# Kernel optimization log

Measured on AMD Instinct MI355X. Metric: run time of the kernel, lower is better.

Reference implementation:

```python
import jax, jax.numpy as jnp
import numpy as np

FEATURE_DIMS = [4, 4, 4, 4, 4, 4, 4, 4, 4, 4, 4, 4, 2, 2, 1, 4, 1, 1, 1, 1, 1, 1, 2]
FEATURE_AMOUNT = len(FEATURE_DIMS)  # 23
EMBEDDING_DIM = 10
KQ_DIM = 10
OBS_SPACE = int(np.sum(FEATURE_DIMS))  # 65
BATCH = 131072


def _block_mask():
    # Block-diagonal mask: feature i's input slice maps only to its own 10-dim embedding.
    m = np.zeros((OBS_SPACE, FEATURE_AMOUNT * EMBEDDING_DIM), dtype=np.float32)
    r = 0
    for i, d in enumerate(FEATURE_DIMS):
        m[r:r + d, i * EMBEDDING_DIM:(i + 1) * EMBEDDING_DIM] = 1.0
        r += d
    return jnp.asarray(m)

PROJ_MASK = _block_mask()


def setup_inputs() -> dict:
    key = jax.random.key(0)
    ks = jax.random.split(key, 24)
    s = 0.1  # weight scale for numerically sane softmax
    inp = {
        "x": jax.random.normal(ks[0], (BATCH, OBS_SPACE), jnp.float32),
        "W_proj": jax.random.normal(ks[1], (OBS_SPACE, FEATURE_AMOUNT * EMBEDDING_DIM), jnp.float32) * s,
        "b_proj": jax.random.normal(ks[2], (FEATURE_AMOUNT * EMBEDDING_DIM,), jnp.float32) * s,
        "Wq": jax.random.normal(ks[3], (EMBEDDING_DIM, KQ_DIM), jnp.float32) * s,
        "Wk": jax.random.normal(ks[4], (EMBEDDING_DIM, KQ_DIM), jnp.float32) * s,
        "Wv": jax.random.normal(ks[5], (EMBEDDING_DIM, EMBEDDING_DIM), jnp.float32) * s,
        "W1": jax.random.normal(ks[6], (FEATURE_AMOUNT * EMBEDDING_DIM, 164), jnp.float32) * s,
        "b1": jax.random.normal(ks[7], (164,), jnp.float32) * s,
        "W2": jax.random.normal(ks[8], (164, 164), jnp.float32) * s,
        "b2": jax.random.normal(ks[9], (164,), jnp.float32) * s,
        "W3": jax.random.normal(ks[10], (164, 164), jnp.float32) * s,
        "b3": jax.random.normal(ks[11], (164,), jnp.float32) * s,
        "W4": jax.random.normal(ks[12], (164, 164), jnp.float32) * s,
        "b4": jax.random.normal(ks[13], (164,), jnp.float32) * s,
        "W5": jax.random.normal(ks[14], (164, 164), jnp.float32) * s,
        "b5": jax.random.normal(ks[15], (164,), jnp.float32) * s,
        "W_move": jax.random.normal(ks[16], (164, 5), jnp.float32) * 0.01,
        "b_move": jax.random.normal(ks[17], (5,), jnp.float32) * s,
        "W_mark": jax.random.normal(ks[18], (164, 1), jnp.float32) * 0.01,
        "b_mark": jax.random.normal(ks[19], (1,), jnp.float32) * s,
    }
    return inp


def reference(x, W_proj, b_proj, Wq, Wk, Wv, W1, b1, W2, b2, W3, b3, W4, b4, W5, b5,
              W_move, b_move, W_mark, b_mark):
    # Projection: 23 tiny Linears fused as one block-diagonal GEMM. [B,65] -> [B,23,10]
    h = (x @ (W_proj * PROJ_MASK) + b_proj).reshape(-1, FEATURE_AMOUNT, EMBEDDING_DIM)
    # Tiny self-attention over the 23 feature tokens.
    q = h @ Wq  # [B,23,kq]
    k = h @ Wk  # [B,23,kq]
    v = h @ Wv  # [B,23,10]
    logits = jnp.einsum('bid,bjd->bij', q, k) / np.float32(np.sqrt(KQ_DIM))
    omega = jax.nn.softmax(logits, axis=-1)
    ctx = jnp.einsum('bij,bjd->bid', omega, v)
    z = (h + ctx).reshape(-1, FEATURE_AMOUNT * EMBEDDING_DIM)  # residual, [B,230]
    # 5-layer MLP, ReLU after every layer (including the last, per source).
    z = jax.nn.relu(z @ W1 + b1)
    z = jax.nn.relu(z @ W2 + b2)
    z = jax.nn.relu(z @ W3 + b3)
    z = jax.nn.relu(z @ W4 + b4)
    z = jax.nn.relu(z @ W5 + b5)
    move = z @ W_move + b_move  # [B,5]
    mark = z @ W_mark + b_mark  # [B,1]
    return (move, mark)
```

## Files before the change

### kernel.cpp

```cpp
#include <hip/hip_runtime.h>

#define BATCH 131072

typedef __attribute__((ext_vector_type(8))) __bf16 bf16x8;
typedef __attribute__((ext_vector_type(16))) float f32x16;
typedef __attribute__((ext_vector_type(2))) float f32x2;

__constant__ int FOFF[23] = {0,4,8,12,16,20,24,28,32,36,40,44,48,50,52,53,57,58,59,60,61,62,63};
__constant__ int FDIM[23] = {4,4,4,4,4,4,4,4,4,4,4,4,2,2,1,4,1,1,1,1,1,1,2};

__device__ __forceinline__ unsigned short f2bf(float f){
  unsigned int u = __float_as_uint(f);
  u += 0x7fffu + ((u>>16)&1u);
  return (unsigned short)(u>>16);
}
__device__ __forceinline__ unsigned int packpair(float a, float b){
  return (unsigned int)f2bf(a) | ((unsigned int)f2bf(b)<<16);
}
__device__ __forceinline__ float bflo(unsigned int u){ return __uint_as_float(u<<16); }
__device__ __forceinline__ float bfhi(unsigned int u){ return __uint_as_float(u & 0xffff0000u); }

__global__ void prep_weights(const float* __restrict__ W1, const float* __restrict__ W2,
    const float* __restrict__ W3, const float* __restrict__ W4, const float* __restrict__ W5,
    unsigned short* __restrict__ wpack){
  int idx = blockIdx.x*256 + threadIdx.x;
  if (idx >= 22656) return;
  const float* W; int rel; int Kd;
  if (idx < 5760){ W = W1; rel = idx; Kd = 230; }
  else {
    int r2 = idx - 5760;
    int li = r2 / 4224; rel = r2 - li*4224; Kd = 164;
    W = (li==0)?W2:((li==1)?W3:((li==2)?W4:W5));
  }
  int lane = rel & 63, rem = rel >> 6;
  int nt = rem % 6, ks = rem / 6;
  int n  = nt*32 + (lane&31);
  int k0 = ks*16 + ((lane>>5)<<3);
  unsigned int v[4];
  #pragma unroll
  for (int p=0;p<4;p++){
    int ka = k0 + 2*p, kb = ka+1;
    float fa = (ka<Kd && n<164) ? W[ka*164+n] : 0.f;
    float fb = (kb<Kd && n<164) ? W[kb*164+n] : 0.f;
    v[p] = packpair(fa, fb);
  }
  *(uint4*)(wpack + (size_t)idx*8) = make_uint4(v[0],v[1],v[2],v[3]);
}

__global__ void prep_small(const float* __restrict__ Wproj, const float* __restrict__ bproj,
    const float* __restrict__ Wq, const float* __restrict__ Wk, const float* __restrict__ Wv,
    const float* __restrict__ Wmove, const float* __restrict__ Wmark,
    unsigned int* __restrict__ swimg){
  int idx = blockIdx.x*256 + threadIdx.x;
  if (idx >= 3064) return;
  unsigned int outv;
  if (idx < 1840){
    int o = idx>>3, u = idx&7;
    int fi = o/10;
    float v = 0.f;
    if (u<4){ if (u < FDIM[fi]) v = Wproj[(FOFF[fi]+u)*230 + o]; }
    else if (u==4) v = bproj[o];
    outv = __float_as_uint(v);
  } else if (idx < 1960){
    int r = idx-1840, e = r/12, d = r-12*e;
    float v = 0.f;
    if (d<10){ float ssum=0.f;
      #pragma unroll
      for (int k2=0;k2<10;k2++) ssum += Wq[e*10+k2]*Wk[d*10+k2];
      v = ssum*0.31622776601683794f; }
    outv = __float_as_uint(v);
  } else if (idx < 2080){
    int r = idx-1960, e = r/12, d = r-12*e;
    outv = __float_as_uint((d<10)? Wv[e*10+d] : 0.f);
  } else {
    int r = idx-2080;
    int o = r/164, k = r-o*164;
    outv = __float_as_uint((o<5)? Wmove[k*5+o] : Wmark[k]);
  }
  swimg[idx] = outv;
}

__device__ __forceinline__ void attn_chunk2(int s, int ibase, int C,
    const f32x2* hf2, const f32x2* swf2, unsigned int* z32){
  f32x2 g2[2][5];
  #pragma unroll
  for (int c=0;c<2;c++)
    #pragma unroll
    for (int p=0;p<5;p++) g2[c][p] = (f32x2){0.f,0.f};
  {
    f32x2 hi2[2][5];
    #pragma unroll
    for (int c=0;c<2;c++) if (c<C){
      #pragma unroll
      for (int p=0;p<5;p++) hi2[c][p] = hf2[((ibase+c)*5+p)*64 + s];
    }
    #pragma unroll
    for (int e=0;e<10;e++){
      f32x2 m2[5];
      #pragma unroll
      for (int p=0;p<5;p++) m2[p] = swf2[920 + e*6 + p];
      #pragma unroll
      for (int c=0;c<2;c++) if (c<C){
        float he = (e&1) ? hi2[c][e>>1].y : hi2[c][e>>1].x;
        #pragma unroll
        for (int p=0;p<5;p++) g2[c][p] += m2[p]*he;
      }
    }
  }
  f32x2 st2[2][5]; float tau[2];
  #pragma unroll
  for (int c=0;c<2;c++){
    tau[c]=0.f;
    #pragma unroll
    for (int p=0;p<5;p++) st2[c][p] = (f32x2){0.f,0.f};
  }
  f32x2 hjA[5], hjB[5];
  auto keystep = [&](f32x2 (&hj)[5]){
    #pragma unroll
    for (int c=0;c<2;c++) if (c<C){
      f32x2 l2 = g2[c][0]*hj[0];
      #pragma unroll
      for (int p=1;p<5;p++) l2 += g2[c][p]*hj[p];
      float e = __expf(l2.x + l2.y);
      tau[c] += e;
      #pragma unroll
      for (int p=0;p<5;p++) st2[c][p] += hj[p]*e;
    }
  };
  #pragma unroll
  for (int p=0;p<5;p++) hjA[p] = hf2[p*64 + s];
  for (int jj=0; jj<11; ++jj){
    #pragma unroll
    for (int p=0;p<5;p++) hjB[p] = hf2[((2*jj+1)*5+p)*64 + s];
    keystep(hjA);
    #pragma unroll
    for (int p=0;p<5;p++) hjA[p] = hf2[((2*jj+2)*5+p)*64 + s];
    keystep(hjB);
  }
  keystep(hjA);
  #pragma unroll
  for (int c=0;c<2;c++) if (c<C){
    float inv = 1.f/tau[c];
    #pragma unroll
    for (int p=0;p<5;p++) st2[c][p] *= inv;
  }
  f32x2 ct2[2][5];
  #pragma unroll
  for (int c=0;c<2;c++)
    #pragma unroll
    for (int p=0;p<5;p++) ct2[c][p] = (f32x2){0.f,0.f};
  #pragma unroll
  for (int e=0;e<10;e++){
    f32x2 wv2[5];
    #pragma unroll
    for (int p=0;p<5;p++) wv2[p] = swf2[980 + e*6 + p];
    #pragma unroll
    for (int c=0;c<2;c++) if (c<C){
      float se = (e&1) ? st2[c][e>>1].y : st2[c][e>>1].x;
      #pragma unroll
      for (int p=0;p<5;p++) ct2[c][p] += wv2[p]*se;
    }
  }
  #pragma unroll
  for (int c=0;c<2;c++) if (c<C){
    int i = ibase+c;
    #pragma unroll
    for (int p=0;p<5;p++){
      f32x2 h = hf2[(i*5+p)*64 + s];
      float z0 = h.x + ct2[c][p].x;
      float z1 = h.y + ct2[c][p].y;
      unsigned int r;
      asm volatile("v_cvt_pk_bf16_f32 %0, %1, %2" : "=v"(r) : "v"(z0), "v"(z1));
      z32[s*124 + i*5 + p] = r;
    }
  }
}

template<int KSTEPS, int NT>
__device__ __forceinline__ void mlp_tiles(const unsigned short* abase, const bf16x8* wb,
    const float* __restrict__ bias, unsigned short* out16, int nt0, int colb, int rowb){
  f32x16 acc[NT];
  #pragma unroll
  for (int nt=0; nt<NT; ++nt)
    #pragma unroll
    for (int r=0;r<16;r++) acc[nt][r]=0.f;
  #pragma unroll
  for (int ks=0; ks<KSTEPS; ++ks){
    bf16x8 a = *(const bf16x8*)(abase + ks*16);
    const bf16x8* wk = wb + ks*(6*64);
    #pragma unroll
    for (int nt=0; nt<NT; ++nt)
      acc[nt] = __builtin_amdgcn_mfma_f32_32x32x16_bf16(a, wk[nt*64], acc[nt], 0,0,0);
  }
  #pragma unroll
  for (int nt=0; nt<NT; ++nt){
    int n = (nt0+nt)*32 + colb;
    float b = (n<164) ? bias[n] : 0.f;
    #pragma unroll
    for (int r=0;r<16;r++){
      int row = rowb + (r&3) + 8*(r>>2);
      float v = fmaxf(acc[nt][r] + b, 0.f);
      out16[row*200 + n] = f2bf(v);
    }
  }
}

template<int KSTEPS>
__device__ __forceinline__ void mlp_layer(const unsigned short* in16, int inPitch,
    const bf16x8* __restrict__ wp, const float* __restrict__ bias,
    unsigned short* out16, int t){
  const int lane = t & 63;
  const int w = t >> 6;
  const int mt = w & 1;
  const int nt = w >> 1;
  if (nt >= 6) return;
  const unsigned short* abase = in16 + (mt*32 + (lane&31))*inPitch + ((lane>>5)<<3);
  const int colb = lane&31;
  const int rowb = mt*32 + 4*(lane>>5);
  mlp_tiles<KSTEPS,1>(abase, wp + nt*64 + lane, bias, out16, nt, colb, rowb);
}

__global__ __launch_bounds__(1024, 1) void actor_main(
    const float* __restrict__ xg,
    const float* __restrict__ b1, const float* __restrict__ b2, const float* __restrict__ b3,
    const float* __restrict__ b4, const float* __restrict__ b5,
    const float* __restrict__ bmove, const float* __restrict__ bmark,
    const unsigned short* __restrict__ wpack, float* __restrict__ out)
{
  __shared__ __align__(16) unsigned char LDS[102880];
  float* xb = (float*)LDS;
  unsigned int* z32 = (unsigned int*)LDS;
  unsigned short* z16 = (unsigned short*)LDS;
  f32x2* hf2 = (f32x2*)(LDS + 31744);
  unsigned short* a16 = (unsigned short*)(LDS + 31744);
  float* sw = (float*)(LDS + 90624);
  unsigned int* swu = (unsigned int*)(LDS + 90624);
  const f32x2* swf2 = (const f32x2*)(LDS + 90624);

  const int t = threadIdx.x;
  const int S0 = blockIdx.x*64;

  {
    const float4* src4 = (const float4*)(xg + (size_t)S0*65);
    float4* x4 = (float4*)LDS;
    for (int i=t; i<1040; i+=1024) x4[i] = src4[i];
    if (t<8) xb[4160+t] = 0.f;
    const unsigned int* swsrc = (const unsigned int*)(wpack + 181248);
    for (int idx=t; idx<3064; idx+=1024) swu[idx] = swsrc[idx];
  }
  __syncthreads();

  for (int L=t; L<7360; L+=1024){
    int s = L & 63, jp = L>>6;
    int j = jp/5, p = jp-5*j;
    int o0 = j*10 + 2*p;
    int roff = FOFF[j];
    float a0 = sw[o0*8+4], a1 = sw[o0*8+12];
    #pragma unroll
    for (int u=0;u<4;u++){
      float xv = xb[s*65 + roff + u];
      a0 += xv * sw[o0*8+u];
      a1 += xv * sw[o0*8+8+u];
    }
    f32x2 hv; hv.x = a0; hv.y = a1;
    hf2[jp*64 + s] = hv;
  }
  __syncthreads();

  {
    const int s = t & 63;
    const int q = t >> 6;
    if (q < 7){
      attn_chunk2(s, 2*q, 2, hf2, swf2, z32);
    } else {
      attn_chunk2(s, q+7, 1, hf2, swf2, z32);
    }
    __builtin_amdgcn_sched_barrier(0);
    if (q == 15){
      for (int idx=s; idx<320; idx+=64){
        int ss = idx/5, pc = idx-5*ss;
        z32[ss*124 + 115+pc] = 0u;
      }
    }
  }
  __syncthreads();

  const bf16x8* wpk = (const bf16x8*)wpack;
  mlp_layer<15>(z16, 248, wpk,          b1, a16, t); __syncthreads();
  mlp_layer<11>(a16, 200, wpk + 5760,   b2, z16, t); __syncthreads();
  mlp_layer<11>(z16, 200, wpk + 9984,   b3, a16, t); __syncthreads();
  mlp_layer<11>(a16, 200, wpk + 14208,  b4, z16, t); __syncthreads();
  mlp_layer<11>(z16, 200, wpk + 18432,  b5, a16, t); __syncthreads();

  {
    float* pb = (float*)LDS;
    if (t < 768){
      int s2 = t & 63, r = t>>6;
      int o = r>>1, half = r&1;
      const uint4* ar4 = (const uint4*)(a16 + s2*200);
      const f32x2* hw = swf2 + 1040 + o*82;
      f32x2 acc2 = {0.f,0.f};
      if (half==0){
        #pragma unroll
        for (int q4=0;q4<10;q4++){
          uint4 v = ar4[q4];
          unsigned int wv[4] = {v.x,v.y,v.z,v.w};
          #pragma unroll
          for (int e=0;e<4;e++){
            f32x2 av; av.x = bflo(wv[e]); av.y = bfhi(wv[e]);
            acc2 += av * hw[q4*4+e];
          }
        }
      } else {
        #pragma unroll
        for (int q4=10;q4<20;q4++){
          uint4 v = ar4[q4];
          unsigned int wv[4] = {v.x,v.y,v.z,v.w};
          #pragma unroll
          for (int e=0;e<4;e++){
            f32x2 av; av.x = bflo(wv[e]); av.y = bfhi(wv[e]);
            acc2 += av * hw[q4*4+e];
          }
        }
        const unsigned int* ar = (const unsigned int*)(a16 + s2*200);
        #pragma unroll
        for (int kp=80;kp<82;kp++){
          unsigned int u = ar[kp];
          f32x2 av; av.x = bflo(u); av.y = bfhi(u);
          acc2 += av * hw[kp];
        }
      }
      pb[r*64 + s2] = acc2.x + acc2.y;
    }
    __syncthreads();
    if (t < 384){
      int s2 = t & 63, o = t>>6;
      float acc = pb[(2*o)*64 + s2] + pb[(2*o+1)*64 + s2];
      acc += (o<5)? bmove[o] : bmark[0];
      if (o<5) out[(size_t)(S0+s2)*5 + o] = acc;
      else     out[(size_t)BATCH*5 + S0 + s2] = acc;
    }
  }
}

extern "C" void kernel_launch(void* const* d_in, const int* in_sizes, int n_in,
                              void* d_out, int out_size, void* d_ws, size_t ws_size,
                              hipStream_t stream){
  (void)in_sizes; (void)n_in; (void)out_size; (void)ws_size;
  const float* x     = (const float*)d_in[0];
  const float* Wproj = (const float*)d_in[1];
  const float* bproj = (const float*)d_in[2];
  const float* Wq    = (const float*)d_in[3];
  const float* Wk    = (const float*)d_in[4];
  const float* Wv    = (const float*)d_in[5];
  const float* W1    = (const float*)d_in[6];
  const float* b1    = (const float*)d_in[7];
  const float* W2    = (const float*)d_in[8];
  const float* b2    = (const float*)d_in[9];
  const float* W3    = (const float*)d_in[10];
  const float* b3    = (const float*)d_in[11];
  const float* W4    = (const float*)d_in[12];
  const float* b4    = (const float*)d_in[13];
  const float* W5    = (const float*)d_in[14];
  const float* b5    = (const float*)d_in[15];
  const float* Wmove = (const float*)d_in[16];
  const float* bmove = (const float*)d_in[17];
  const float* Wmark = (const float*)d_in[18];
  const float* bmark = (const float*)d_in[19];
  unsigned short* wpack = (unsigned short*)d_ws;
  unsigned int* swimg = (unsigned int*)(wpack + 181248);

  prep_weights<<<89, 256, 0, stream>>>(W1, W2, W3, W4, W5, wpack);
  prep_small<<<12, 256, 0, stream>>>(Wproj, bproj, Wq, Wk, Wv, Wmove, Wmark, swimg);
  actor_main<<<2048, 1024, 0, stream>>>(x,
      b1, b2, b3, b4, b5, bmove, bmark, wpack, (float*)d_out);
}
```

Measured before the change: 265.3 us.

## Halve per-block sample tile to 32 so three blocks fit per CU

Each block now handles 32 samples with 512 threads instead of 64 samples with 1024 threads, and LDS drops from about 100KB to about 50KB. Launch bounds change to 512 threads with 3 blocks per CU. The projection weights are moved into the otherwise idle space after the x tile, so the small-weight region now holds only the attention and head weights. Each MLP wave computes a single 32-row M tile. The aim is more resident blocks per CU, so one block's barrier-separated phases can overlap another block's work. The cost is that every block still reloads the same weights for half as many samples.

```diff
diff --git a/kernel.cpp b/kernel.cpp
--- a/kernel.cpp
+++ b/kernel.cpp
@@ -92,13 +92,13 @@
     #pragma unroll
     for (int c=0;c<2;c++) if (c<C){
       #pragma unroll
-      for (int p=0;p<5;p++) hi2[c][p] = hf2[((ibase+c)*5+p)*64 + s];
+      for (int p=0;p<5;p++) hi2[c][p] = hf2[((ibase+c)*5+p)*32 + s];
     }
     #pragma unroll
     for (int e=0;e<10;e++){
       f32x2 m2[5];
       #pragma unroll
-      for (int p=0;p<5;p++) m2[p] = swf2[920 + e*6 + p];
+      for (int p=0;p<5;p++) m2[p] = swf2[e*6 + p];
       #pragma unroll
       for (int c=0;c<2;c++) if (c<C){
         float he = (e&1) ? hi2[c][e>>1].y : hi2[c][e>>1].x;
@@ -128,13 +128,13 @@
     }
   };
   #pragma unroll
-  for (int p=0;p<5;p++) hjA[p] = hf2[p*64 + s];
+  for (int p=0;p<5;p++) hjA[p] = hf2[p*32 + s];
   for (int jj=0; jj<11; ++jj){
     #pragma unroll
-    for (int p=0;p<5;p++) hjB[p] = hf2[((2*jj+1)*5+p)*64 + s];
+    for (int p=0;p<5;p++) hjB[p] = hf2[((2*jj+1)*5+p)*32 + s];
     keystep(hjA);
     #pragma unroll
-    for (int p=0;p<5;p++) hjA[p] = hf2[((2*jj+2)*5+p)*64 + s];
+    for (int p=0;p<5;p++) hjA[p] = hf2[((2*jj+2)*5+p)*32 + s];
     keystep(hjB);
   }
   keystep(hjA);
@@ -153,7 +153,7 @@
   for (int e=0;e<10;e++){
     f32x2 wv2[5];
     #pragma unroll
-    for (int p=0;p<5;p++) wv2[p] = swf2[980 + e*6 + p];
+    for (int p=0;p<5;p++) wv2[p] = swf2[60 + e*6 + p];
     #pragma unroll
     for (int c=0;c<2;c++) if (c<C){
       float se = (e&1) ? st2[c][e>>1].y : st2[c][e>>1].x;
@@ -166,7 +166,7 @@
     int i = ibase+c;
     #pragma unroll
     for (int p=0;p<5;p++){
-      f32x2 h = hf2[(i*5+p)*64 + s];
+      f32x2 h = hf2[(i*5+p)*32 + s];
       float z0 = h.x + ct2[c][p].x;
       float z1 = h.y + ct2[c][p].y;
       unsigned int r;
@@ -176,111 +176,97 @@
   }
 }
 
-template<int KSTEPS, int NT>
-__device__ __forceinline__ void mlp_tiles(const unsigned short* abase, const bf16x8* wb,
-    const float* __restrict__ bias, unsigned short* out16, int nt0, int colb, int rowb){
-  f32x16 acc[NT];
-  #pragma unroll
-  for (int nt=0; nt<NT; ++nt)
-    #pragma unroll
-    for (int r=0;r<16;r++) acc[nt][r]=0.f;
-  #pragma unroll
-  for (int ks=0; ks<KSTEPS; ++ks){
-    bf16x8 a = *(const bf16x8*)(abase + ks*16);
-    const bf16x8* wk = wb + ks*(6*64);
-    #pragma unroll
-    for (int nt=0; nt<NT; ++nt)
-      acc[nt] = __builtin_amdgcn_mfma_f32_32x32x16_bf16(a, wk[nt*64], acc[nt], 0,0,0);
-  }
-  #pragma unroll
-  for (int nt=0; nt<NT; ++nt){
-    int n = (nt0+nt)*32 + colb;
-    float b = (n<164) ? bias[n] : 0.f;
-    #pragma unroll
-    for (int r=0;r<16;r++){
-      int row = rowb + (r&3) + 8*(r>>2);
-      float v = fmaxf(acc[nt][r] + b, 0.f);
-      out16[row*200 + n] = f2bf(v);
-    }
-  }
-}
-
 template<int KSTEPS>
 __device__ __forceinline__ void mlp_layer(const unsigned short* in16, int inPitch,
     const bf16x8* __restrict__ wp, const float* __restrict__ bias,
     unsigned short* out16, int t){
   const int lane = t & 63;
-  const int w = t >> 6;
-  const int mt = w & 1;
-  const int nt = w >> 1;
+  const int nt = t >> 6;
   if (nt >= 6) return;
-  const unsigned short* abase = in16 + (mt*32 + (lane&31))*inPitch + ((lane>>5)<<3);
+  const unsigned short* abase = in16 + (lane&31)*inPitch + ((lane>>5)<<3);
+  const bf16x8* wb = wp + nt*64 + lane;
+  f32x16 acc;
+  #pragma unroll
+  for (int r=0;r<16;r++) acc[r]=0.f;
+  #pragma unroll
+  for (int ks=0; ks<KSTEPS; ++ks){
+    bf16x8 a = *(const bf16x8*)(abase + ks*16);
+    acc = __builtin_amdgcn_mfma_f32_32x32x16_bf16(a, wb[ks*(6*64)], acc, 0,0,0);
+  }
   const int colb = lane&31;
-  const int rowb = mt*32 + 4*(lane>>5);
-  mlp_tiles<KSTEPS,1>(abase, wp + nt*64 + lane, bias, out16, nt, colb, rowb);
-}
-
-__global__ __launch_bounds__(1024, 1) void actor_main(
+  const int rowb = 4*(lane>>5);
+  int n = nt*32 + colb;
+  float b = (n<164) ? bias[n] : 0.f;
+  #pragma unroll
+  for (int r=0;r<16;r++){
+    int row = rowb + (r&3) + 8*(r>>2);
+    float v = fmaxf(acc[r] + b, 0.f);
+    out16[row*200 + n] = f2bf(v);
+  }
+}
+
+__global__ __launch_bounds__(512, 3) void actor_main(
     const float* __restrict__ xg,
     const float* __restrict__ b1, const float* __restrict__ b2, const float* __restrict__ b3,
     const float* __restrict__ b4, const float* __restrict__ b5,
     const float* __restrict__ bmove, const float* __restrict__ bmark,
     const unsigned short* __restrict__ wpack, float* __restrict__ out)
 {
-  __shared__ __align__(16) unsigned char LDS[102880];
+  __shared__ __align__(16) unsigned char LDS[50208];
   float* xb = (float*)LDS;
+  unsigned int* xw = (unsigned int*)LDS;
   unsigned int* z32 = (unsigned int*)LDS;
   unsigned short* z16 = (unsigned short*)LDS;
-  f32x2* hf2 = (f32x2*)(LDS + 31744);
-  unsigned short* a16 = (unsigned short*)(LDS + 31744);
-  float* sw = (float*)(LDS + 90624);
-  unsigned int* swu = (unsigned int*)(LDS + 90624);
-  const f32x2* swf2 = (const f32x2*)(LDS + 90624);
+  f32x2* hf2 = (f32x2*)(LDS + 15872);
+  unsigned short* a16 = (unsigned short*)(LDS + 15872);
+  float* swp = (float*)(LDS + 45312);
+  const f32x2* swf2 = (const f32x2*)(LDS + 45312);
 
   const int t = threadIdx.x;
-  const int S0 = blockIdx.x*64;
+  const int S0 = blockIdx.x*32;
 
   {
     const float4* src4 = (const float4*)(xg + (size_t)S0*65);
     float4* x4 = (float4*)LDS;
-    for (int i=t; i<1040; i+=1024) x4[i] = src4[i];
-    if (t<8) xb[4160+t] = 0.f;
+    for (int i=t; i<520; i+=512) x4[i] = src4[i];
+    if (t<8) xb[2080+t] = 0.f;
     const unsigned int* swsrc = (const unsigned int*)(wpack + 181248);
-    for (int idx=t; idx<3064; idx+=1024) swu[idx] = swsrc[idx];
+    for (int idx=t; idx<1840; idx+=512) xw[2088+idx] = swsrc[idx];
+    for (int idx=t; idx<1224; idx+=512)
+      ((unsigned int*)swp)[idx] = swsrc[1840+idx];
   }
   __syncthreads();
 
-  for (int L=t; L<7360; L+=1024){
-    int s = L & 63, jp = L>>6;
+  const float* pw = xb + 2088;
+  for (int L=t; L<3680; L+=512){
+    int s = L & 31, jp = L>>5;
     int j = jp/5, p = jp-5*j;
     int o0 = j*10 + 2*p;
     int roff = FOFF[j];
-    float a0 = sw[o0*8+4], a1 = sw[o0*8+12];
+    float a0 = pw[o0*8+4], a1 = pw[o0*8+12];
     #pragma unroll
     for (int u=0;u<4;u++){
       float xv = xb[s*65 + roff + u];
-      a0 += xv * sw[o0*8+u];
-      a1 += xv * sw[o0*8+8+u];
+      a0 += xv * pw[o0*8+u];
+      a1 += xv * pw[o0*8+8+u];
     }
     f32x2 hv; hv.x = a0; hv.y = a1;
-    hf2[jp*64 + s] = hv;
+    hf2[jp*32 + s] = hv;
   }
   __syncthreads();
 
   {
-    const int s = t & 63;
-    const int q = t >> 6;
+    const int s = t & 31;
+    const int q = t >> 5;
     if (q < 7){
       attn_chunk2(s, 2*q, 2, hf2, swf2, z32);
     } else {
       attn_chunk2(s, q+7, 1, hf2, swf2, z32);
     }
     __builtin_amdgcn_sched_barrier(0);
-    if (q == 15){
-      for (int idx=s; idx<320; idx+=64){
-        int ss = idx/5, pc = idx-5*ss;
-        z32[ss*124 + 115+pc] = 0u;
-      }
+    for (int idx=t; idx<160; idx+=512){
+      int ss = idx/5, pc = idx-5*ss;
+      z32[ss*124 + 115+pc] = 0u;
     }
   }
   __syncthreads();
@@ -294,11 +280,11 @@
 
   {
     float* pb = (float*)LDS;
-    if (t < 768){
-      int s2 = t & 63, r = t>>6;
+    if (t < 384){
+      int s2 = t & 31, r = t>>5;
       int o = r>>1, half = r&1;
       const uint4* ar4 = (const uint4*)(a16 + s2*200);
-      const f32x2* hw = swf2 + 1040 + o*82;
+      const f32x2* hw = swf2 + 120 + o*82;
       f32x2 acc2 = {0.f,0.f};
       if (half==0){
         #pragma unroll
@@ -330,12 +316,12 @@
           acc2 += av * hw[kp];
         }
       }
-      pb[r*64 + s2] = acc2.x + acc2.y;
+      pb[r*32 + s2] = acc2.x + acc2.y;
     }
     __syncthreads();
-    if (t < 384){
-      int s2 = t & 63, o = t>>6;
-      float acc = pb[(2*o)*64 + s2] + pb[(2*o+1)*64 + s2];
+    if (t < 192){
+      int s2 = t & 31, o = t>>5;
+      float acc = pb[(2*o)*32 + s2] + pb[(2*o+1)*32 + s2];
       acc += (o<5)? bmove[o] : bmark[0];
       if (o<5) out[(size_t)(S0+s2)*5 + o] = acc;
       else     out[(size_t)BATCH*5 + S0 + s2] = acc;
@@ -372,6 +358,6 @@
 
   prep_weights<<<89, 256, 0, stream>>>(W1, W2, W3, W4, W5, wpack);
   prep_small<<<12, 256, 0, stream>>>(Wproj, bproj, Wq, Wk, Wv, Wmove, Wmark, swimg);
-  actor_main<<<2048, 1024, 0, stream>>>(x,
+  actor_main<<<4096, 512, 0, stream>>>(x,
       b1, b2, b3, b4, b5, bmove, bmark, wpack, (float*)d_out);
 }
```

Measured after the change: 258.2 us. 1.03x faster.
